# Performance work log

Measured on AMD Instinct MI355X. Metric: run time of the kernel, lower is better.

Reference implementation:

```python
import jax, jax.numpy as jnp
import numpy as np

R = 2
K = 2 * R + 1  # kernel size 5


def _patches(x, axis):
    """Zero-padded sliding-window patches along `axis` for a [B,H,W,1] tensor.
    Mimics tf.image.extract_patches with SAME padding (zeros). Returns [B,H,W,K]."""
    pad = [(0, 0)] * 4
    pad[axis] = (R, R)
    xp = jnp.pad(x, pad)
    n = x.shape[axis]
    slices = [jax.lax.slice_in_dim(xp, i, i + n, axis=axis) for i in range(K)]
    return jnp.concatenate(slices, axis=-1)  # channel dim is 1 -> stacks taps


def _do_blur(bright_p, dark_p, depths_p, depths, spatial_dist, depth_var, spatial_var):
    # depth-guided weight, per tap
    rel = jnp.minimum(jnp.abs(depths_p / depths - 1.0), 1.0)
    w = jnp.exp(-jnp.square(rel) / (2.0 * depth_var)) * \
        jnp.exp(-jnp.square(spatial_dist) / (2.0 * spatial_var))
    w = w / jnp.sum(w, axis=-1, keepdims=True)
    b = jnp.sum(bright_p * w, axis=-1, keepdims=True)
    d = jnp.sum(dark_p * w, axis=-1, keepdims=True)
    return b, d


def _custom_pow(a, b):
    return jnp.exp(b * jnp.log(jnp.maximum(a, 1e-8)))


def setup_inputs() -> dict:
    key = jax.random.key(0)
    k1, k2, k3 = jax.random.split(key, 3)
    B, H, W = 8, 1024, 1024
    bright = jax.random.uniform(k1, (B, H, W, 1), dtype=jnp.float32)
    dark = jax.random.uniform(k2, (B, H, W, 1), dtype=jnp.float32)
    # depths are divided by; keep strictly positive
    depths = 0.1 + 0.9 * jax.random.uniform(k3, (B, H, W, 1), dtype=jnp.float32)
    return {
        "bright": bright,
        "dark": dark,
        "depths": depths,
        "depth_variance": jnp.float32(0.0004),
        "spatial_variance": jnp.float32(13.16),
        "dev_exponent": jnp.float32(0.3),
        "dark_epsilon": jnp.float32(0.375),
        "contrast_enhance": jnp.float32(0.95),
    }


def reference(bright, dark, depths, depth_variance, spatial_variance,
              dev_exponent, dark_epsilon, contrast_enhance):
    spatial_dist = jnp.arange(-R, R + 1, dtype=jnp.float32).reshape(1, 1, 1, K)
    # horizontal pass (along W = axis 2)
    bx, dx, zx = _patches(bright, 2), _patches(dark, 2), _patches(depths, 2)
    bright_x, dark_x = _do_blur(bx, dx, zx, depths, spatial_dist,
                                depth_variance, spatial_variance)
    # vertical pass (along H = axis 1) on horizontally-blurred values
    by, dy, zy = _patches(bright_x, 1), _patches(dark_x, 1), _patches(depths, 1)
    bright_mean, dark_mean = _do_blur(by, dy, zy, depths, spatial_dist,
                                      depth_variance, spatial_variance)
    # contrast-aware blend of bright/dark channels
    dev_bright = _custom_pow(jnp.abs(bright - bright_mean), dev_exponent)
    dev_dark = _custom_pow(jnp.abs(dark - dark_mean), dev_exponent)
    dev_dark = jnp.maximum(dev_dark, dark_epsilon)
    dev_bright = dev_bright * contrast_enhance
    wsum = dev_bright + dev_dark
    dev_bright = dev_bright / wsum
    dev_dark = dev_dark / wsum
    return dev_dark * bright + dev_bright * dark
```

## Files before the change

kernel.cpp:

```cpp
#include <hip/hip_runtime.h>
#include <stdint.h>

#define TH 8
#define W_ 1024
#define H_ 1024

typedef __attribute__((address_space(3))) uint32_t lds_u32;
typedef __attribute__((address_space(1))) const uint32_t glb_u32;

__device__ __forceinline__ void dma16(const float* g, float* l) {
    __builtin_amdgcn_global_load_lds((glb_u32*)(uintptr_t)g,
                                     (lds_u32*)(uintptr_t)l, 16, 0, 0);
}

__device__ __forceinline__ float wexp1(float zp, float iz, float kd, float kspat) {
    const float u = fmaf(zp, iz, -1.0f);
    return __builtin_amdgcn_exp2f(fmaf(u * kd, u, kspat));
}

__device__ __forceinline__ void blur5(
    float zm2, float zm1, float zc, float zp1, float zp2,
    float bm2, float bm1, float bc, float bp1, float bp2,
    float dm2, float dm1, float dc, float dp1, float dp2,
    float kd, float ks1, float ks4,
    float& ob, float& od)
{
    const float iz = __builtin_amdgcn_rcpf(zc);
    const float w0 = wexp1(zm2, iz, kd, ks4);
    const float w1 = wexp1(zm1, iz, kd, ks1);
    const float w3 = wexp1(zp1, iz, kd, ks1);
    const float w4 = wexp1(zp2, iz, kd, ks4);
    const float wr = __builtin_amdgcn_rcpf(1.0f + w0 + w1 + w3 + w4);
    ob = fmaf(w0, bm2, fmaf(w1, bm1, fmaf(w3, bp1, fmaf(w4, bp2, bc)))) * wr;
    od = fmaf(w0, dm2, fmaf(w1, dm1, fmaf(w3, dp1, fmaf(w4, dp2, dc)))) * wr;
}

__device__ __forceinline__ float blend1(float bc, float dc, float bm, float dm,
                                        float de, float dke, float ce) {
    const float devb = __builtin_amdgcn_exp2f(
        de * __builtin_amdgcn_logf(fmaxf(fabsf(bc - bm), 1e-8f))) * ce;
    const float devd = fmaxf(__builtin_amdgcn_exp2f(
        de * __builtin_amdgcn_logf(fmaxf(fabsf(dc - dm), 1e-8f))), dke);
    const float wr = __builtin_amdgcn_rcpf(devb + devd);
    return fmaf(devd, bc, devb * dc) * wr;
}

__device__ __forceinline__ void dma_row(
    int gy, const float* __restrict__ bB, const float* __restrict__ dB,
    const float* __restrict__ zB,
    float* sZs, float* sBs, float* sDs, int c, int wb)
{
    const int gyc = min(max(gy, 0), H_ - 1);
    const size_t ro = (size_t)gyc * W_;
    dma16(zB + ro + c, sZs + wb);
    dma16(bB + ro + c, sBs + wb);
    dma16(dB + ro + c, sDs + wb);
}

__device__ __forceinline__ void hblur_lds(
    int gy, const float* sZs, const float* sBs, const float* sDs,
    int c, int colL2, int colR2, bool eL, bool eR,
    float kd, float ks1, float ks4,
    float4& sb, float4& sd, float4& sz)
{
    if ((unsigned)gy < (unsigned)H_) {
        float2 lz = *(const float2*)(sZs + colL2);
        const float4 cz = *(const float4*)(sZs + c);
        float2 rz = *(const float2*)(sZs + colR2);
        const float2 lb = *(const float2*)(sBs + colL2);
        const float4 cb = *(const float4*)(sBs + c);
        const float2 rb = *(const float2*)(sBs + colR2);
        const float2 ld = *(const float2*)(sDs + colL2);
        const float4 cd = *(const float4*)(sDs + c);
        const float2 rd = *(const float2*)(sDs + colR2);
        if (eL) { lz.x = 1e18f; lz.y = 1e18f; }
        if (eR) { rz.x = 1e18f; rz.y = 1e18f; }
        blur5(lz.x, lz.y, cz.x, cz.y, cz.z,  lb.x, lb.y, cb.x, cb.y, cb.z,
              ld.x, ld.y, cd.x, cd.y, cd.z,  kd, ks1, ks4, sb.x, sd.x);
        blur5(lz.y, cz.x, cz.y, cz.z, cz.w,  lb.y, cb.x, cb.y, cb.z, cb.w,
              ld.y, cd.x, cd.y, cd.z, cd.w,  kd, ks1, ks4, sb.y, sd.y);
        blur5(cz.x, cz.y, cz.z, cz.w, rz.x,  cb.x, cb.y, cb.z, cb.w, rb.x,
              cd.x, cd.y, cd.z, cd.w, rd.x,  kd, ks1, ks4, sb.z, sd.z);
        blur5(cz.y, cz.z, cz.w, rz.x, rz.y,  cb.y, cb.z, cb.w, rb.x, rb.y,
              cd.y, cd.z, cd.w, rd.x, rd.y,  kd, ks1, ks4, sb.w, sd.w);
        sz = cz;
    } else {
        sb = make_float4(0.f, 0.f, 0.f, 0.f);
        sd = make_float4(0.f, 0.f, 0.f, 0.f);
        sz = make_float4(0.f, 0.f, 0.f, 0.f);
    }
}

#define PHASE(N)                                                              \
    asm volatile("s_waitcnt vmcnt(" #N ")" ::: "memory");                     \
    __builtin_amdgcn_s_barrier();                                             \
    asm volatile("" ::: "memory");

#define WSTEP(S, CS, DS, K, N)                                                \
  {                                                                           \
    dma_row(y0 + (K) - 1, bB, dB, zB, sZ[DS], sB[DS], sD[DS], c, wb);         \
    PHASE(N)                                                                  \
    hblur_lds(y0 + (K) - 2, sZ[CS], sB[CS], sD[CS], c, colL2, colR2, eL, eR,  \
              kd, ks1, ks4, pb[S], pd[S], pz[S]);                             \
  }

#define FSTEP(S, S0, S1, S2, S3, S4, CS, DS, K, N, DODMA)                     \
  {                                                                           \
    const size_t oo = (size_t)(y0 + (K) - 4) * W_ + c;                        \
    const float4 rb4 = *(const float4*)(bB + oo);                             \
    const float4 rd4 = *(const float4*)(dB + oo);                             \
    asm volatile("" ::: "memory");  \
    if (DODMA) dma_row(y0 + (K) - 1, bB, dB, zB, sZ[DS], sB[DS], sD[DS], c, wb); \
    PHASE(N)                                                                  \
    hblur_lds(y0 + (K) - 2, sZ[CS], sB[CS], sD[CS], c, colL2, colR2, eL, eR,  \
              kd, ks1, ks4, pb[S], pd[S], pz[S]);                             \
    float4 bm, dm;                                                            \
    blur5(pz[S0].x, pz[S1].x, pz[S2].x, pz[S3].x, pz[S4].x,                   \
          pb[S0].x, pb[S1].x, pb[S2].x, pb[S3].x, pb[S4].x,                   \
          pd[S0].x, pd[S1].x, pd[S2].x, pd[S3].x, pd[S4].x,                   \
          kd, ks1, ks4, bm.x, dm.x);                                          \
    blur5(pz[S0].y, pz[S1].y, pz[S2].y, pz[S3].y, pz[S4].y,                   \
          pb[S0].y, pb[S1].y, pb[S2].y, pb[S3].y, pb[S4].y,                   \
          pd[S0].y, pd[S1].y, pd[S2].y, pd[S3].y, pd[S4].y,                   \
          kd, ks1, ks4, bm.y, dm.y);                                          \
    blur5(pz[S0].z, pz[S1].z, pz[S2].z, pz[S3].z, pz[S4].z,                   \
          pb[S0].z, pb[S1].z, pb[S2].z, pb[S3].z, pb[S4].z,                   \
          pd[S0].z, pd[S1].z, pd[S2].z, pd[S3].z, pd[S4].z,                   \
          kd, ks1, ks4, bm.z, dm.z);                                          \
    blur5(pz[S0].w, pz[S1].w, pz[S2].w, pz[S3].w, pz[S4].w,                   \
          pb[S0].w, pb[S1].w, pb[S2].w, pb[S3].w, pb[S4].w,                   \
          pd[S0].w, pd[S1].w, pd[S2].w, pd[S3].w, pd[S4].w,                   \
          kd, ks1, ks4, bm.w, dm.w);                                          \
    float4 res;                                                               \
    res.x = blend1(rb4.x, rd4.x, bm.x, dm.x, de, dke, ce);                    \
    res.y = blend1(rb4.y, rd4.y, bm.y, dm.y, de, dke, ce);                    \
    res.z = blend1(rb4.z, rd4.z, bm.z, dm.z, de, dke, ce);                    \
    res.w = blend1(rb4.w, rd4.w, bm.w, dm.w, de, dke, ce);                    \
    *(float4*)(outB + oo) = res;                                              \
  }

__global__ __launch_bounds__(256, 4)
void bilateral_fused(const float* __restrict__ bright,
                     const float* __restrict__ dark,
                     const float* __restrict__ depths,
                     const float* __restrict__ p_dv,
                     const float* __restrict__ p_sv,
                     const float* __restrict__ p_de,
                     const float* __restrict__ p_deps,
                     const float* __restrict__ p_ce,
                     float* __restrict__ out)
{
    __shared__ __attribute__((aligned(16))) float sZ[3][W_];
    __shared__ __attribute__((aligned(16))) float sB[3][W_];
    __shared__ __attribute__((aligned(16))) float sD[3][W_];

    const float LOG2E = 1.44269504088896340736f;
    const float kd  = -LOG2E / (2.0f * p_dv[0]);
    const float ks  = -LOG2E / (2.0f * p_sv[0]);
    const float de  = p_de[0];
    const float dke = p_deps[0];
    const float ce  = p_ce[0];
    const float ks1 = ks;
    const float ks4 = 4.0f * ks;

    const int t  = threadIdx.x;
    const int c  = 4 * t;
    const int wb = (t >> 6) << 8;
    const int y0 = blockIdx.y * TH;

    const size_t plane = (size_t)H_ * W_;
    const float* bB = bright + (size_t)blockIdx.z * plane;
    const float* dB = dark   + (size_t)blockIdx.z * plane;
    const float* zB = depths + (size_t)blockIdx.z * plane;
    float*     outB = out    + (size_t)blockIdx.z * plane;

    const int  colL2 = max(c - 2, 0);
    const int  colR2 = min(c + 4, W_ - 2);
    const bool eL = (c == 0);
    const bool eR = (c + 4 >= W_);

    float4 pb[5], pd[5], pz[5];

    dma_row(y0 - 2, bB, dB, zB, sZ[0], sB[0], sD[0], c, wb);

    WSTEP(0, 0, 1, 0, 3)
    WSTEP(1, 1, 2, 1, 3)
    WSTEP(2, 2, 0, 2, 3)
    WSTEP(3, 0, 1, 3, 3)

    FSTEP(4, 0, 1, 2, 3, 4,  1, 2,  4, 5, 1)
    FSTEP(0, 1, 2, 3, 4, 0,  2, 0,  5, 6, 1)
    FSTEP(1, 2, 3, 4, 0, 1,  0, 1,  6, 6, 1)
    FSTEP(2, 3, 4, 0, 1, 2,  1, 2,  7, 6, 1)
    FSTEP(3, 4, 0, 1, 2, 3,  2, 0,  8, 6, 1)
    FSTEP(4, 0, 1, 2, 3, 4,  0, 1,  9, 6, 1)
    FSTEP(0, 1, 2, 3, 4, 0,  1, 2, 10, 6, 1)
    FSTEP(1, 2, 3, 4, 0, 1,  2, 0, 11, 3, 0)
}

extern "C" void kernel_launch(void* const* d_in, const int* in_sizes, int n_in,
                              void* d_out, int out_size, void* d_ws, size_t ws_size,
                              hipStream_t stream)
{
    const float* bright = (const float*)d_in[0];
    const float* dark   = (const float*)d_in[1];
    const float* depths = (const float*)d_in[2];
    const float* p_dv   = (const float*)d_in[3];
    const float* p_sv   = (const float*)d_in[4];
    const float* p_de   = (const float*)d_in[5];
    const float* p_deps = (const float*)d_in[6];
    const float* p_ce   = (const float*)d_in[7];
    float* out = (float*)d_out;

    const int B = in_sizes[0] / (H_ * W_);

    dim3 grid(1, H_ / TH, B);
    dim3 block(256);
    bilateral_fused<<<grid, block, 0, stream>>>(bright, dark, depths,
                                                p_dv, p_sv, p_de, p_deps, p_ce,
                                                out);
}
```

Before: 161.2 us.

## Make each wave's LDS row slice private and drop block barriers via halo loads

Each wave now reads only the 256-column LDS slice it DMA'd itself. The two-column halo at each wave boundary is fetched directly from global memory into registers. This removes every s_barrier, leaving only per-wave vmcnt waits, and shrinks the LDS ring from three row buffers to two, which lowers LDS use per block. The cost is six extra small global loads per row and more outstanding memory ops per wave. The correctness of the double buffering now depends on in-order vmcnt accounting within a single wave.

```diff
diff --git a/kernel.cpp b/kernel.cpp
--- a/kernel.cpp
+++ b/kernel.cpp
@@ -12,6 +12,8 @@
     __builtin_amdgcn_global_load_lds((glb_u32*)(uintptr_t)g,
                                      (lds_u32*)(uintptr_t)l, 16, 0, 0);
 }
+
+#define FENCE() asm volatile("" ::: "memory")
 
 __device__ __forceinline__ float wexp1(float zp, float iz, float kd, float kspat) {
     const float u = fmaf(zp, iz, -1.0f);
@@ -45,6 +47,22 @@
     return fmaf(devd, bc, devb * dc) * wr;
 }
 
+struct Halo { float2 lz, rz, lb, rb, ld, rd; };
+
+__device__ __forceinline__ void halo_load(
+    int gy, const float* __restrict__ bB, const float* __restrict__ dB,
+    const float* __restrict__ zB, int hl, int hr, Halo& h)
+{
+    const int gyc = min(max(gy, 0), H_ - 1);
+    const size_t ro = (size_t)gyc * W_;
+    h.lz = *(const float2*)(zB + ro + hl);
+    h.rz = *(const float2*)(zB + ro + hr);
+    h.lb = *(const float2*)(bB + ro + hl);
+    h.rb = *(const float2*)(bB + ro + hr);
+    h.ld = *(const float2*)(dB + ro + hl);
+    h.rd = *(const float2*)(dB + ro + hr);
+}
+
 __device__ __forceinline__ void dma_row(
     int gy, const float* __restrict__ bB, const float* __restrict__ dB,
     const float* __restrict__ zB,
@@ -57,22 +75,26 @@
     dma16(dB + ro + c, sDs + wb);
 }
 
-__device__ __forceinline__ void hblur_lds(
+__device__ __forceinline__ void hblur_priv(
     int gy, const float* sZs, const float* sBs, const float* sDs,
-    int c, int colL2, int colR2, bool eL, bool eR,
+    int c, int tl, int wb, const Halo& h, bool eL, bool eR,
     float kd, float ks1, float ks4,
     float4& sb, float4& sd, float4& sz)
 {
     if ((unsigned)gy < (unsigned)H_) {
-        float2 lz = *(const float2*)(sZs + colL2);
+        const int cL = max(c - 2, wb);
+        const int cR = min(c + 4, wb + 252);
+        float2 lz = *(const float2*)(sZs + cL);
         const float4 cz = *(const float4*)(sZs + c);
-        float2 rz = *(const float2*)(sZs + colR2);
-        const float2 lb = *(const float2*)(sBs + colL2);
+        float2 rz = *(const float2*)(sZs + cR);
+        float2 lb = *(const float2*)(sBs + cL);
         const float4 cb = *(const float4*)(sBs + c);
-        const float2 rb = *(const float2*)(sBs + colR2);
-        const float2 ld = *(const float2*)(sDs + colL2);
+        float2 rb = *(const float2*)(sBs + cR);
+        float2 ld = *(const float2*)(sDs + cL);
         const float4 cd = *(const float4*)(sDs + c);
-        const float2 rd = *(const float2*)(sDs + colR2);
+        float2 rd = *(const float2*)(sDs + cR);
+        if (tl == 0)  { lz = h.lz; lb = h.lb; ld = h.ld; }
+        if (tl == 63) { rz = h.rz; rb = h.rb; rd = h.rd; }
         if (eL) { lz.x = 1e18f; lz.y = 1e18f; }
         if (eR) { rz.x = 1e18f; rz.y = 1e18f; }
         blur5(lz.x, lz.y, cz.x, cz.y, cz.z,  lb.x, lb.y, cb.x, cb.y, cb.z,
@@ -91,29 +113,32 @@
     }
 }
 
-#define PHASE(N)                                                              \
-    asm volatile("s_waitcnt vmcnt(" #N ")" ::: "memory");                     \
-    __builtin_amdgcn_s_barrier();                                             \
-    asm volatile("" ::: "memory");
-
-#define WSTEP(S, CS, DS, K, N)                                                \
+#define WSTEP(S, SC, SD, I)                                                   \
   {                                                                           \
-    dma_row(y0 + (K) - 1, bB, dB, zB, sZ[DS], sB[DS], sD[DS], c, wb);         \
-    PHASE(N)                                                                  \
-    hblur_lds(y0 + (K) - 2, sZ[CS], sB[CS], sD[CS], c, colL2, colR2, eL, eR,  \
-              kd, ks1, ks4, pb[S], pd[S], pz[S]);                             \
+    Halo h;                                                                   \
+    halo_load(y0 + (I) - 2, bB, dB, zB, hl, hr, h);                           \
+    FENCE();                                                                  \
+    dma_row(y0 + (I) - 1, bB, dB, zB, sZ[SD], sB[SD], sD[SD], c, wb);         \
+    FENCE();                                                                  \
+    asm volatile("s_waitcnt vmcnt(9)" ::: "memory");                          \
+    hblur_priv(y0 + (I) - 2, sZ[SC], sB[SC], sD[SC], c, tl, wb, h, eL, eR,    \
+               kd, ks1, ks4, pb[S], pd[S], pz[S]);                            \
   }
 
-#define FSTEP(S, S0, S1, S2, S3, S4, CS, DS, K, N, DODMA)                     \
+#define FSTEP(S, S0, S1, S2, S3, S4, SC, SD, I, VN, DODMA)                    \
   {                                                                           \
-    const size_t oo = (size_t)(y0 + (K) - 4) * W_ + c;                        \
+    Halo h;                                                                   \
+    halo_load(y0 + (I) - 2, bB, dB, zB, hl, hr, h);                           \
+    FENCE();                                                                  \
+    if (DODMA) dma_row(y0 + (I) - 1, bB, dB, zB, sZ[SD], sB[SD], sD[SD], c, wb); \
+    FENCE();                                                                  \
+    const size_t oo = (size_t)(y0 + (I) - 4) * W_ + c;                        \
     const float4 rb4 = *(const float4*)(bB + oo);                             \
     const float4 rd4 = *(const float4*)(dB + oo);                             \
-    asm volatile("" ::: "memory");  \
-    if (DODMA) dma_row(y0 + (K) - 1, bB, dB, zB, sZ[DS], sB[DS], sD[DS], c, wb); \
-    PHASE(N)                                                                  \
-    hblur_lds(y0 + (K) - 2, sZ[CS], sB[CS], sD[CS], c, colL2, colR2, eL, eR,  \
-              kd, ks1, ks4, pb[S], pd[S], pz[S]);                             \
+    FENCE();                                                                  \
+    asm volatile("s_waitcnt vmcnt(" #VN ")" ::: "memory");                    \
+    hblur_priv(y0 + (I) - 2, sZ[SC], sB[SC], sD[SC], c, tl, wb, h, eL, eR,    \
+               kd, ks1, ks4, pb[S], pd[S], pz[S]);                            \
     float4 bm, dm;                                                            \
     blur5(pz[S0].x, pz[S1].x, pz[S2].x, pz[S3].x, pz[S4].x,                   \
           pb[S0].x, pb[S1].x, pb[S2].x, pb[S3].x, pb[S4].x,                   \
@@ -150,9 +175,9 @@
                      const float* __restrict__ p_ce,
                      float* __restrict__ out)
 {
-    __shared__ __attribute__((aligned(16))) float sZ[3][W_];
-    __shared__ __attribute__((aligned(16))) float sB[3][W_];
-    __shared__ __attribute__((aligned(16))) float sD[3][W_];
+    __shared__ __attribute__((aligned(16))) float sZ[2][W_];
+    __shared__ __attribute__((aligned(16))) float sB[2][W_];
+    __shared__ __attribute__((aligned(16))) float sD[2][W_];
 
     const float LOG2E = 1.44269504088896340736f;
     const float kd  = -LOG2E / (2.0f * p_dv[0]);
@@ -164,8 +189,9 @@
     const float ks4 = 4.0f * ks;
 
     const int t  = threadIdx.x;
+    const int tl = t & 63;
     const int c  = 4 * t;
-    const int wb = (t >> 6) << 8;
+    const int wb = c & ~255;
     const int y0 = blockIdx.y * TH;
 
     const size_t plane = (size_t)H_ * W_;
@@ -174,8 +200,8 @@
     const float* zB = depths + (size_t)blockIdx.z * plane;
     float*     outB = out    + (size_t)blockIdx.z * plane;
 
-    const int  colL2 = max(c - 2, 0);
-    const int  colR2 = min(c + 4, W_ - 2);
+    const int  hl = max(wb - 2, 0);
+    const int  hr = min(wb + 256, W_ - 2);
     const bool eL = (c == 0);
     const bool eR = (c + 4 >= W_);
 
@@ -183,19 +209,19 @@
 
     dma_row(y0 - 2, bB, dB, zB, sZ[0], sB[0], sD[0], c, wb);
 
-    WSTEP(0, 0, 1, 0, 3)
-    WSTEP(1, 1, 2, 1, 3)
-    WSTEP(2, 2, 0, 2, 3)
-    WSTEP(3, 0, 1, 3, 3)
-
-    FSTEP(4, 0, 1, 2, 3, 4,  1, 2,  4, 5, 1)
-    FSTEP(0, 1, 2, 3, 4, 0,  2, 0,  5, 6, 1)
-    FSTEP(1, 2, 3, 4, 0, 1,  0, 1,  6, 6, 1)
-    FSTEP(2, 3, 4, 0, 1, 2,  1, 2,  7, 6, 1)
-    FSTEP(3, 4, 0, 1, 2, 3,  2, 0,  8, 6, 1)
-    FSTEP(4, 0, 1, 2, 3, 4,  0, 1,  9, 6, 1)
-    FSTEP(0, 1, 2, 3, 4, 0,  1, 2, 10, 6, 1)
-    FSTEP(1, 2, 3, 4, 0, 1,  2, 0, 11, 3, 0)
+    WSTEP(0, 0, 1, 0)
+    WSTEP(1, 1, 0, 1)
+    WSTEP(2, 0, 1, 2)
+    WSTEP(3, 1, 0, 3)
+
+    FSTEP(4, 0, 1, 2, 3, 4,  0, 1,  4, 11, 1)
+    FSTEP(0, 1, 2, 3, 4, 0,  1, 0,  5, 12, 1)
+    FSTEP(1, 2, 3, 4, 0, 1,  0, 1,  6, 12, 1)
+    FSTEP(2, 3, 4, 0, 1, 2,  1, 0,  7, 12, 1)
+    FSTEP(3, 4, 0, 1, 2, 3,  0, 1,  8, 12, 1)
+    FSTEP(4, 0, 1, 2, 3, 4,  1, 0,  9, 12, 1)
+    FSTEP(0, 1, 2, 3, 4, 0,  0, 1, 10, 12, 1)
+    FSTEP(1, 2, 3, 4, 0, 1,  1, 0, 11,  9, 0)
 }
 
 extern "C" void kernel_launch(void* const* d_in, const int* in_sizes, int n_in,
```

Result: slower. 182.5 us (+13.3%).
